# Performance work log

Measured on AMD Instinct MI355X. Metric: run time of the kernel, lower is better.

Reference implementation:

```python
import jax, jax.numpy as jnp
import numpy as np

EPS = 1e-7  # tf.keras.backend.epsilon()
ITERATIONS = 3

def squash(t, axis=-1):
    n2 = jnp.sum(jnp.square(t), axis=axis, keepdims=True)
    scale = n2 / (1.0 + n2) / jnp.sqrt(n2 + EPS)
    return scale * t

def setup_inputs() -> dict:
    key = jax.random.key(0)
    k1, k2 = jax.random.split(key)
    B, N_in, K_in = 64, 1152, 8
    N_out, K_out = 64, 16
    x = jax.random.normal(k1, (B, N_in, K_in), dtype=jnp.float32)
    W = jax.random.normal(k2, (N_out, N_in, K_out, K_in), dtype=jnp.float32) * 0.05
    return {"x": x, "W": W}

def reference(x, W):
    # x: [B, N_in, K_in]; W: [N_out, N_in, K_out, K_in]
    # prediction vectors u: [B, N_out, N_in, K_out]
    u = jnp.einsum('oikj,bij->boik', W, x)
    B, N_out, N_in, K_out = u.shape
    b = jnp.zeros((B, N_out, N_in), dtype=u.dtype)
    v = None
    for i in range(ITERATIONS):
        c = jax.nn.softmax(b, axis=1)            # softmax over N_out
        s = jnp.einsum('boi,boik->bok', c, u)    # [B, N_out, K_out]
        v = squash(s, axis=-1)
        if i < ITERATIONS - 1:
            b = b + jnp.einsum('bok,boik->boi', v, u)
    return v  # [B, N_out, K_out]
```

## Files before the change

kernel.cpp:

```cpp
#include <hip/hip_runtime.h>
#include <math.h>


#define CTI 18
#define IPB 2
#define NSTEP 9
#define CNCH 64

typedef __attribute__((ext_vector_type(8))) short short8v;
typedef __attribute__((ext_vector_type(8))) unsigned short ushort8v;
typedef __attribute__((ext_vector_type(4))) float f32x4;

typedef const __attribute__((address_space(1))) unsigned int gu32;
typedef __attribute__((address_space(3))) unsigned int lu32;

__device__ __forceinline__ unsigned short f2bf(float f) {
    unsigned u = __builtin_bit_cast(unsigned, f);
    u = u + 0x7FFFu + ((u >> 16) & 1u);
    return (unsigned short)(u >> 16);
}
__device__ __forceinline__ float bf2f(unsigned short h) {
    unsigned u = ((unsigned)h) << 16;
    return __builtin_bit_cast(float, u);
}
__device__ __forceinline__ float lo16f(unsigned u) {
    return __builtin_bit_cast(float, u << 16);
}
__device__ __forceinline__ float hi16f(unsigned u) {
    return __builtin_bit_cast(float, u & 0xFFFF0000u);
}

__global__ __launch_bounds__(256)
void xform(const float* __restrict__ W, const float* __restrict__ x,
           unsigned short* __restrict__ Wp, unsigned short* __restrict__ xpp) {
    const int bid = blockIdx.x;
    if (bid < 4608) {
        int tid = bid * 256 + threadIdx.x;
        int k = tid & 15, o = (tid >> 4) & 63, i = tid >> 10;
        const float4* src = (const float4*)(W + (((size_t)o * 1152 + i) * 16 + k) * 8);
        float4 v0 = src[0], v1 = src[1];
        float vf[8] = {v0.x, v0.y, v0.z, v0.w, v1.x, v1.y, v1.z, v1.w};
        ushort8v hi, lo;
        #pragma unroll
        for (int j = 0; j < 8; ++j) {
            unsigned short h = f2bf(vf[j]);
            hi[j] = h;
            lo[j] = f2bf(vf[j] - bf2f(h));
        }
        size_t base = (((size_t)i * 64 + o) * 2) * 128 + (size_t)k * 8;
        *reinterpret_cast<ushort8v*>(Wp + base)       = hi;
        *reinterpret_cast<ushort8v*>(Wp + base + 128) = lo;
    } else {
        int tid = (bid - 4608) * 256 + threadIdx.x;
        int b = tid & 63, i = tid >> 6;
        const float4* src = (const float4*)(x + ((size_t)b * 1152 + i) * 8);
        float4 v0 = src[0], v1 = src[1];
        float vf[8] = {v0.x, v0.y, v0.z, v0.w, v1.x, v1.y, v1.z, v1.w};
        ushort8v hi, lo;
        #pragma unroll
        for (int j = 0; j < 8; ++j) {
            unsigned short h = f2bf(vf[j]);
            hi[j] = h;
            lo[j] = f2bf(vf[j] - bf2f(h));
        }
        size_t base = ((size_t)i * 2) * 512 + (size_t)b * 8;
        *reinterpret_cast<ushort8v*>(xpp + base)       = hi;
        *reinterpret_cast<ushort8v*>(xpp + base + 512) = lo;
    }
}

template<int ROUTED>
__global__ __launch_bounds__(1024, 1)
void caps_mfma(const unsigned short* __restrict__ Wp,
               const unsigned short* __restrict__ xp,
               const float* __restrict__ Vfp,
               unsigned short* __restrict__ spart) {
    __shared__ unsigned short wlds[2][IPB * 16384];
    __shared__ float zbuf[2][IPB][256];

    const int t = threadIdx.x;
    const int wv = t >> 6, l = t & 63;
    const int btile = blockIdx.x >> 6, chunk = blockIdx.x & 63;
    const int g = l >> 4, b15 = l & 15;
    const int o0 = wv * 4;
    const int i0 = chunk * CTI;

    uint2 vpk[4];
    if (ROUTED) {
        #pragma unroll
        for (int oo = 0; oo < 4; ++oo) {
            f32x4 Vf = *reinterpret_cast<const f32x4*>(
                Vfp + (((size_t)btile * 64 + o0 + oo) * 64 + l) * 4);
            vpk[oo].x = (unsigned)f2bf(Vf[0]) | ((unsigned)f2bf(Vf[1]) << 16);
            vpk[oo].y = (unsigned)f2bf(Vf[2]) | ((unsigned)f2bf(Vf[3]) << 16);
        }
    }

    f32x4 s[4];
    #pragma unroll
    for (int oo = 0; oo < 4; ++oo) s[oo] = (f32x4){0.f, 0.f, 0.f, 0.f};

    #define STAGE2(buf, ibase)                                                    \
    {                                                                             \
        const ushort8v* srcb = reinterpret_cast<const ushort8v*>(                 \
            Wp + (size_t)(ibase) * 16384);                                        \
        _Pragma("unroll")                                                         \
        for (int r = 0; r < 4; ++r)                                               \
            __builtin_amdgcn_global_load_lds(                                     \
                (gu32*)(srcb + (r * 1024 + wv * 64 + l)),                         \
                (lu32*)&wlds[buf][(size_t)(r * 1024 + wv * 64) * 8], 16, 0, 0);   \
    }

    #define LOADB(i) (*reinterpret_cast<const short8v*>(                          \
        xp + (((size_t)(i) * 2 + (l >> 5)) * 64 + btile * 16 + b15) * 8))

    STAGE2(0, i0);
    short8v Bf0 = LOADB(i0);
    short8v Bf1 = LOADB(i0 + 1);
    __syncthreads();

    int cur = 0;
    for (int st = 0; st < NSTEP; ++st) {
        short8v Bn0 = Bf0, Bn1 = Bf1;
        if (st + 1 < NSTEP) {
            STAGE2(cur ^ 1, i0 + (st + 1) * IPB);
            Bn0 = LOADB(i0 + (st + 1) * IPB);
            Bn1 = LOADB(i0 + (st + 1) * IPB + 1);
        }

        if (!ROUTED) {
            #pragma unroll
            for (int oo = 0; oo < 4; ++oo) {
                short8v Af0 = *reinterpret_cast<const short8v*>(
                    &wlds[cur][0] + (((o0 + oo) * 2 + (g & 1)) * 128 + b15 * 8));
                s[oo] = __builtin_amdgcn_mfma_f32_16x16x32_bf16(Af0, Bf0, s[oo], 0, 0, 0);
                short8v Af1 = *reinterpret_cast<const short8v*>(
                    &wlds[cur][16384] + (((o0 + oo) * 2 + (g & 1)) * 128 + b15 * 8));
                s[oo] = __builtin_amdgcn_mfma_f32_16x16x32_bf16(Af1, Bf1, s[oo], 0, 0, 0);
            }
            __syncthreads();
        } else {
            f32x4 u[IPB][4];
            float lg[IPB][4];
            float Zp0 = 0.f, Zp1 = 0.f;
            #pragma unroll
            for (int oo = 0; oo < 4; ++oo) {
                short8v Af0 = *reinterpret_cast<const short8v*>(
                    &wlds[cur][0] + (((o0 + oo) * 2 + (g & 1)) * 128 + b15 * 8));
                f32x4 zz = {0.f, 0.f, 0.f, 0.f};
                u[0][oo] = __builtin_amdgcn_mfma_f32_16x16x32_bf16(Af0, Bf0, zz, 0, 0, 0);
                short8v Af1 = *reinterpret_cast<const short8v*>(
                    &wlds[cur][16384] + (((o0 + oo) * 2 + (g & 1)) * 128 + b15 * 8));
                u[1][oo] = __builtin_amdgcn_mfma_f32_16x16x32_bf16(Af1, Bf1, zz, 0, 0, 0);

                float p0 = u[0][oo][0] * lo16f(vpk[oo].x);
                p0 = fmaf(u[0][oo][1], hi16f(vpk[oo].x), p0);
                p0 = fmaf(u[0][oo][2], lo16f(vpk[oo].y), p0);
                p0 = fmaf(u[0][oo][3], hi16f(vpk[oo].y), p0);
                float p1 = u[1][oo][0] * lo16f(vpk[oo].x);
                p1 = fmaf(u[1][oo][1], hi16f(vpk[oo].x), p1);
                p1 = fmaf(u[1][oo][2], lo16f(vpk[oo].y), p1);
                p1 = fmaf(u[1][oo][3], hi16f(vpk[oo].y), p1);
                p0 += __shfl_xor(p0, 16, 64);  p1 += __shfl_xor(p1, 16, 64);
                p0 += __shfl_xor(p0, 32, 64);  p1 += __shfl_xor(p1, 32, 64);
                float e0 = __expf(p0), e1 = __expf(p1);
                lg[0][oo] = e0; lg[1][oo] = e1;
                Zp0 += e0; Zp1 += e1;
            }
            if (l < 16) {
                zbuf[st & 1][0][wv * 16 + l] = Zp0;
                zbuf[st & 1][1][wv * 16 + l] = Zp1;
            }
            __syncthreads();
            float Z0 = zbuf[st & 1][0][b15];
            float Z1 = zbuf[st & 1][1][b15];
            #pragma unroll
            for (int w2 = 1; w2 < 16; ++w2) {
                Z0 += zbuf[st & 1][0][w2 * 16 + b15];
                Z1 += zbuf[st & 1][1][w2 * 16 + b15];
            }
            float rz0 = 1.0f / Z0, rz1 = 1.0f / Z1;
            #pragma unroll
            for (int oo = 0; oo < 4; ++oo) {
                float c0 = lg[0][oo] * rz0;
                float c1 = lg[1][oo] * rz1;
                s[oo][0] = fmaf(c0, u[0][oo][0], fmaf(c1, u[1][oo][0], s[oo][0]));
                s[oo][1] = fmaf(c0, u[0][oo][1], fmaf(c1, u[1][oo][1], s[oo][1]));
                s[oo][2] = fmaf(c0, u[0][oo][2], fmaf(c1, u[1][oo][2], s[oo][2]));
                s[oo][3] = fmaf(c0, u[0][oo][3], fmaf(c1, u[1][oo][3], s[oo][3]));
            }
        }
        Bf0 = Bn0; Bf1 = Bn1;
        cur ^= 1;
    }

    const float fin = ROUTED ? 1.0f : (1.0f / 64.0f);
    #pragma unroll
    for (int oo = 0; oo < 4; ++oo) {
        f32x4 vv = s[oo] * fin;
        uint2 pk;
        pk.x = (unsigned)f2bf(vv[0]) | ((unsigned)f2bf(vv[1]) << 16);
        pk.y = (unsigned)f2bf(vv[2]) | ((unsigned)f2bf(vv[3]) << 16);
        *reinterpret_cast<uint2*>(spart +
            ((((size_t)chunk * 4 + btile) * 64 + (o0 + oo)) * 64 + l) * 4) = pk;
    }
    #undef STAGE2
    #undef LOADB
}

template<int MODE>
__global__ __launch_bounds__(256)
void reduce2(const unsigned short* __restrict__ spart, float* __restrict__ Vfp,
             float* __restrict__ out) {
    __shared__ f32x4 red[256];
    const int t = threadIdx.x;
    const int l = t & 63, cq = t >> 6;
    const int pair = blockIdx.x;
    const int btile = pair >> 6, o = pair & 63;

    f32x4 acc = {0.f, 0.f, 0.f, 0.f};
    const unsigned short* base = spart + (((size_t)btile * 64 + o) * 64 + l) * 4;
    for (int c = cq * (CNCH/4); c < (cq + 1) * (CNCH/4); ++c) {
        uint2 w = *reinterpret_cast<const uint2*>(base + (size_t)c * 65536);
        acc[0] += lo16f(w.x); acc[1] += hi16f(w.x);
        acc[2] += lo16f(w.y); acc[3] += hi16f(w.y);
    }
    red[t] = acc;
    __syncthreads();
    if (cq == 0) {
        acc = red[l] + red[64 + l] + red[128 + l] + red[192 + l];
        float n2 = acc[0]*acc[0] + acc[1]*acc[1] + acc[2]*acc[2] + acc[3]*acc[3];
        n2 += __shfl_xor(n2, 16, 64);
        n2 += __shfl_xor(n2, 32, 64);
        const float scale = n2 / (1.0f + n2) / sqrtf(n2 + 1e-7f);
        f32x4 v = acc * scale;
        float* vp = Vfp + (((size_t)btile * 64 + o) * 64 + l) * 4;
        if (MODE == 0) {
            *reinterpret_cast<f32x4*>(vp) = v;
        } else if (MODE == 1) {
            f32x4 old = *reinterpret_cast<const f32x4*>(vp);
            *reinterpret_cast<f32x4*>(vp) = old + v;
        } else {
            const int b = btile * 16 + (l & 15), gq = l >> 4;
            *reinterpret_cast<f32x4*>(out + (((size_t)b * 64 + o) * 16 + gq * 4)) = v;
        }
    }
}

#define FTI 18
#define FNCH 64

__device__ __forceinline__ void load_lds16(const float4* gp, float4* lp) {
    __builtin_amdgcn_global_load_lds((gu32*)gp, (lu32*)lp, 16, 0, 0);
}
__device__ __forceinline__ float rfl(float v) {
    return __builtin_bit_cast(float, __builtin_amdgcn_readfirstlane(__builtin_bit_cast(int, v)));
}

template<bool UNIFORM>
__global__ __launch_bounds__(256, 2)
void caps_route_fb(const float* __restrict__ x, const float* __restrict__ W,
                   const float* __restrict__ Vsum, float* __restrict__ s_out) {
    __shared__ float4 wlds[2][2048];
    __shared__ float4 xlds[8 * FTI * 2];
    const int t = threadIdx.x;
    const int w = t >> 6, o = t & 63;
    const int chunk = blockIdx.x % FNCH, bblk = blockIdx.x / FNCH;
    const int i0 = chunk * FTI, bbase = bblk * 8 + w * 2;
    const float4* __restrict__ xg = (const float4*)x;
    const float4* __restrict__ Wg = (const float4*)W;
    for (int e = t; e < 8 * FTI * 2; e += 256) {
        int bb = e / (FTI * 2), r = e % (FTI * 2);
        xlds[e] = xg[((bblk * 8 + bb) * 1152 + i0 + (r >> 1)) * 2 + (r & 1)];
    }
    const float4* wsrc = Wg + (size_t)o * 36864 + (size_t)i0 * 32 + w * 8;
    #pragma unroll
    for (int r = 0; r < 8; ++r) load_lds16(wsrc + r, &wlds[0][(w * 8 + r) * 64]);
    float vsf[2][16];
    if (!UNIFORM) {
        const float4* vg = (const float4*)Vsum;
        #pragma unroll
        for (int ll = 0; ll < 2; ++ll)
            #pragma unroll
            for (int q = 0; q < 4; ++q) {
                float4 v = vg[((size_t)(bbase + ll) * 64 + o) * 4 + q];
                vsf[ll][q*4+0] = v.x; vsf[ll][q*4+1] = v.y;
                vsf[ll][q*4+2] = v.z; vsf[ll][q*4+3] = v.w;
            }
    }
    float sacc[2][16];
    #pragma unroll
    for (int ll = 0; ll < 2; ++ll)
        #pragma unroll
        for (int k = 0; k < 16; ++k) sacc[ll][k] = 0.0f;
    for (int ii = 0; ii < FTI; ++ii) {
        const int cur = ii & 1;
        __syncthreads();
        if (ii + 1 < FTI) {
            const float4* ws = wsrc + (size_t)(ii + 1) * 32;
            #pragma unroll
            for (int r = 0; r < 8; ++r) load_lds16(ws + r, &wlds[cur ^ 1][(w * 8 + r) * 64]);
        }
        float4 A0 = xlds[(w*2+0)*(FTI*2) + ii*2 + 0];
        float4 B0 = xlds[(w*2+0)*(FTI*2) + ii*2 + 1];
        float4 A1 = xlds[(w*2+1)*(FTI*2) + ii*2 + 0];
        float4 B1 = xlds[(w*2+1)*(FTI*2) + ii*2 + 1];
        float xa0x=rfl(A0.x),xa0y=rfl(A0.y),xa0z=rfl(A0.z),xa0w=rfl(A0.w);
        float xb0x=rfl(B0.x),xb0y=rfl(B0.y),xb0z=rfl(B0.z),xb0w=rfl(B0.w);
        float xa1x=rfl(A1.x),xa1y=rfl(A1.y),xa1z=rfl(A1.z),xa1w=rfl(A1.w);
        float xb1x=rfl(B1.x),xb1y=rfl(B1.y),xb1z=rfl(B1.z),xb1w=rfl(B1.w);
        const float4* wb = wlds[cur];
        float u[2][16];
        float logit0 = 0.0f, logit1 = 0.0f;
        #pragma unroll
        for (int k = 0; k < 16; ++k) {
            float4 w0 = wb[(2*k  )*64 + o];
            float4 w1 = wb[(2*k+1)*64 + o];
            float uk0 = w0.x*xa0x; uk0=fmaf(w0.y,xa0y,uk0); uk0=fmaf(w0.z,xa0z,uk0);
            uk0=fmaf(w0.w,xa0w,uk0); uk0=fmaf(w1.x,xb0x,uk0); uk0=fmaf(w1.y,xb0y,uk0);
            uk0=fmaf(w1.z,xb0z,uk0); uk0=fmaf(w1.w,xb0w,uk0);
            float uk1 = w0.x*xa1x; uk1=fmaf(w0.y,xa1y,uk1); uk1=fmaf(w0.z,xa1z,uk1);
            uk1=fmaf(w0.w,xa1w,uk1); uk1=fmaf(w1.x,xb1x,uk1); uk1=fmaf(w1.y,xb1y,uk1);
            uk1=fmaf(w1.z,xb1z,uk1); uk1=fmaf(w1.w,xb1w,uk1);
            u[0][k]=uk0; u[1][k]=uk1;
            if (!UNIFORM) { logit0=fmaf(vsf[0][k],uk0,logit0); logit1=fmaf(vsf[1][k],uk1,logit1); }
        }
        float c0, c1;
        if (UNIFORM) { c0 = c1 = 1.0f/64.0f; }
        else {
            float m0=logit0, m1=logit1;
            #pragma unroll
            for (int d=32; d>=1; d>>=1) { m0=fmaxf(m0,__shfl_xor(m0,d,64)); m1=fmaxf(m1,__shfl_xor(m1,d,64)); }
            float e0=__expf(logit0-m0), e1=__expf(logit1-m1);
            float s0=e0, s1=e1;
            #pragma unroll
            for (int d=32; d>=1; d>>=1) { s0+=__shfl_xor(s0,d,64); s1+=__shfl_xor(s1,d,64); }
            c0=e0/s0; c1=e1/s1;
        }
        #pragma unroll
        for (int k = 0; k < 16; ++k) {
            sacc[0][k]=fmaf(c0,u[0][k],sacc[0][k]);
            sacc[1][k]=fmaf(c1,u[1][k],sacc[1][k]);
        }
    }
    #pragma unroll
    for (int ll = 0; ll < 2; ++ll) {
        float4* sp = (float4*)s_out + (((size_t)chunk * 64 + (bbase + ll)) * 64 + o) * 4;
        sp[0]=make_float4(sacc[ll][0],sacc[ll][1],sacc[ll][2],sacc[ll][3]);
        sp[1]=make_float4(sacc[ll][4],sacc[ll][5],sacc[ll][6],sacc[ll][7]);
        sp[2]=make_float4(sacc[ll][8],sacc[ll][9],sacc[ll][10],sacc[ll][11]);
        sp[3]=make_float4(sacc[ll][12],sacc[ll][13],sacc[ll][14],sacc[ll][15]);
    }
}

template<int MODE>
__global__ __launch_bounds__(256)
void reduce_squash_fb(const float* __restrict__ sp, float* __restrict__ Vs, float* __restrict__ out) {
    const int t = threadIdx.x;
    const int p = t >> 4, q = t & 15;
    const int pair = blockIdx.x * 16 + p;
    const int b = pair >> 6, o = pair & 63;
    float acc[16];
    #pragma unroll
    for (int k = 0; k < 16; ++k) acc[k] = 0.0f;
    const float4* base = (const float4*)sp;
    for (int c = q * (FNCH/16); c < (q + 1) * (FNCH/16); ++c) {
        const float4* pptr = base + (((size_t)c * 64 + b) * 64 + o) * 4;
        float4 v0=pptr[0],v1=pptr[1],v2=pptr[2],v3=pptr[3];
        acc[0]+=v0.x;acc[1]+=v0.y;acc[2]+=v0.z;acc[3]+=v0.w;
        acc[4]+=v1.x;acc[5]+=v1.y;acc[6]+=v1.z;acc[7]+=v1.w;
        acc[8]+=v2.x;acc[9]+=v2.y;acc[10]+=v2.z;acc[11]+=v2.w;
        acc[12]+=v3.x;acc[13]+=v3.y;acc[14]+=v3.z;acc[15]+=v3.w;
    }
    #pragma unroll
    for (int d = 1; d < 16; d <<= 1)
        #pragma unroll
        for (int k = 0; k < 16; ++k) acc[k] += __shfl_xor(acc[k], d, 64);
    if (q == 0) {
        float n2 = 0.0f;
        #pragma unroll
        for (int k = 0; k < 16; ++k) n2 = fmaf(acc[k], acc[k], n2);
        const float scale = n2 / (1.0f + n2) / sqrtf(n2 + 1e-7f);
        if (MODE == 0) {
            float4* vf = (float4*)Vs + (size_t)pair * 4;
            #pragma unroll
            for (int r = 0; r < 4; ++r)
                vf[r] = make_float4(scale*acc[r*4+0],scale*acc[r*4+1],scale*acc[r*4+2],scale*acc[r*4+3]);
        } else if (MODE == 1) {
            float4* vf = (float4*)Vs + (size_t)pair * 4;
            #pragma unroll
            for (int r = 0; r < 4; ++r) {
                float4 v = vf[r];
                v.x=fmaf(scale,acc[r*4+0],v.x); v.y=fmaf(scale,acc[r*4+1],v.y);
                v.z=fmaf(scale,acc[r*4+2],v.z); v.w=fmaf(scale,acc[r*4+3],v.w);
                vf[r] = v;
            }
        } else {
            float4* of = (float4*)out + (size_t)pair * 4;
            #pragma unroll
            for (int r = 0; r < 4; ++r)
                of[r] = make_float4(scale*acc[r*4+0],scale*acc[r*4+1],scale*acc[r*4+2],scale*acc[r*4+3]);
        }
    }
}

extern "C" void kernel_launch(void* const* d_in, const int* in_sizes, int n_in,
                              void* d_out, int out_size, void* d_ws, size_t ws_size,
                              hipStream_t stream) {
    const float* x = (const float*)d_in[0];
    const float* W = (const float*)d_in[1];
    float* out = (float*)d_out;

    float* Vfp = (float*)d_ws;
    unsigned short* spart = (unsigned short*)(Vfp + 65536);
    unsigned short* Wp = spart + (size_t)CNCH * 65536;
    unsigned short* xpp = Wp + (size_t)1152 * 64 * 256;
    const size_t need_full = (size_t)65536 * 4
        + ((size_t)CNCH * 65536 + (size_t)1152 * 64 * 256 + (size_t)1152 * 2 * 512) * 2;

    if (ws_size >= need_full) {
        xform<<<4608 + 288, 256, 0, stream>>>(W, x, Wp, xpp);
        caps_mfma<0><<<256, 1024, 0, stream>>>(Wp, xpp, Vfp, spart);
        reduce2<0><<<256, 256, 0, stream>>>(spart, Vfp, out);
        caps_mfma<1><<<256, 1024, 0, stream>>>(Wp, xpp, Vfp, spart);
        reduce2<1><<<256, 256, 0, stream>>>(spart, Vfp, out);
        caps_mfma<1><<<256, 1024, 0, stream>>>(Wp, xpp, Vfp, spart);
        reduce2<2><<<256, 256, 0, stream>>>(spart, Vfp, out);
    } else {
        float* Vs = (float*)d_ws;
        float* sp = Vs + 65536;
        dim3 grid(8 * FNCH), blk(256);
        dim3 rg(256), rb(256);
        caps_route_fb<true ><<<grid, blk, 0, stream>>>(x, W, nullptr, sp);
        reduce_squash_fb<0><<<rg, rb, 0, stream>>>(sp, Vs, out);
        caps_route_fb<false><<<grid, blk, 0, stream>>>(x, W, Vs, sp);
        reduce_squash_fb<1><<<rg, rb, 0, stream>>>(sp, Vs, out);
        caps_route_fb<false><<<grid, blk, 0, stream>>>(x, W, Vs, sp);
        reduce_squash_fb<2><<<rg, rb, 0, stream>>>(sp, Vs, out);
    }
}
```

Baseline: 91.49 us.

## Fuse all routing passes into one cooperative kernel with grid syncs

Measured after the change: 309.4 us. 3.38x slower.

```diff
diff --git a/kernel.cpp b/kernel.cpp
--- a/kernel.cpp
+++ b/kernel.cpp
@@ -1,5 +1,8 @@
 #include <hip/hip_runtime.h>
+#include <hip/hip_cooperative_groups.h>
 #include <math.h>
+
+namespace cg = cooperative_groups;
 
 
 #define CTI 18
@@ -28,6 +31,230 @@
 }
 __device__ __forceinline__ float hi16f(unsigned u) {
     return __builtin_bit_cast(float, u & 0xFFFF0000u);
+}
+
+__global__ __launch_bounds__(1024, 1)
+void caps_fused(const float* __restrict__ W, const float* __restrict__ x,
+                unsigned short* __restrict__ Wp, unsigned short* __restrict__ xp,
+                float* __restrict__ Vfp, unsigned short* __restrict__ spart,
+                float* __restrict__ out) {
+    cg::grid_group grid = cg::this_grid();
+
+    __shared__ alignas(16) unsigned short wlds[2][IPB * 16384];
+    __shared__ float zbuf[2][IPB][256];
+
+    const int t = threadIdx.x;
+    const int wv = t >> 6, l = t & 63;
+    const int btile = blockIdx.x >> 6, chunk = blockIdx.x & 63;
+    const int g = l >> 4, b15 = l & 15;
+    const int o0 = wv * 4;
+    const int i0 = chunk * CTI;
+
+    {
+        const int gtid = blockIdx.x * 1024 + t;
+        for (int idx = gtid; idx < 1152 * 64 * 16; idx += 256 * 1024) {
+            int k = idx & 15, o = (idx >> 4) & 63, i = idx >> 10;
+            const float4* src = (const float4*)(W + (((size_t)o * 1152 + i) * 16 + k) * 8);
+            float4 v0 = src[0], v1 = src[1];
+            float vf[8] = {v0.x, v0.y, v0.z, v0.w, v1.x, v1.y, v1.z, v1.w};
+            ushort8v hi, lo;
+            #pragma unroll
+            for (int j = 0; j < 8; ++j) {
+                unsigned short h = f2bf(vf[j]);
+                hi[j] = h;
+                lo[j] = f2bf(vf[j] - bf2f(h));
+            }
+            size_t base = (((size_t)i * 64 + o) * 2) * 128 + (size_t)k * 8;
+            *reinterpret_cast<ushort8v*>(Wp + base)       = hi;
+            *reinterpret_cast<ushort8v*>(Wp + base + 128) = lo;
+        }
+        for (int idx = gtid; idx < 1152 * 64; idx += 256 * 1024) {
+            int b = idx & 63, i = idx >> 6;
+            const float4* src = (const float4*)(x + ((size_t)b * 1152 + i) * 8);
+            float4 v0 = src[0], v1 = src[1];
+            float vf[8] = {v0.x, v0.y, v0.z, v0.w, v1.x, v1.y, v1.z, v1.w};
+            ushort8v hi, lo;
+            #pragma unroll
+            for (int j = 0; j < 8; ++j) {
+                unsigned short h = f2bf(vf[j]);
+                hi[j] = h;
+                lo[j] = f2bf(vf[j] - bf2f(h));
+            }
+            size_t base = ((size_t)i * 2) * 512 + (size_t)b * 8;
+            *reinterpret_cast<ushort8v*>(xp + base)       = hi;
+            *reinterpret_cast<ushort8v*>(xp + base + 512) = lo;
+        }
+    }
+
+    #define STAGE2(buf, ibase)                                                    \
+    {                                                                             \
+        const ushort8v* srcb = reinterpret_cast<const ushort8v*>(                 \
+            Wp + (size_t)(ibase) * 16384);                                        \
+        _Pragma("unroll")                                                         \
+        for (int r = 0; r < 4; ++r)                                               \
+            __builtin_amdgcn_global_load_lds(                                     \
+                (gu32*)(srcb + (r * 1024 + wv * 64 + l)),                         \
+                (lu32*)&wlds[buf][(size_t)(r * 1024 + wv * 64) * 8], 16, 0, 0);   \
+    }
+    #define LOADB(i) (*reinterpret_cast<const short8v*>(                          \
+        xp + (((size_t)(i) * 2 + (l >> 5)) * 64 + btile * 16 + b15) * 8))
+
+    #define CAPS_PASS(R)                                                          \
+    {                                                                             \
+        uint2 vpk[4];                                                             \
+        if (R) {                                                                  \
+            _Pragma("unroll")                                                     \
+            for (int oo = 0; oo < 4; ++oo) {                                      \
+                f32x4 Vf = *reinterpret_cast<const f32x4*>(                       \
+                    Vfp + (((size_t)btile * 64 + o0 + oo) * 64 + l) * 4);         \
+                vpk[oo].x = (unsigned)f2bf(Vf[0]) | ((unsigned)f2bf(Vf[1]) << 16);\
+                vpk[oo].y = (unsigned)f2bf(Vf[2]) | ((unsigned)f2bf(Vf[3]) << 16);\
+            }                                                                     \
+        }                                                                         \
+        f32x4 s[4];                                                               \
+        _Pragma("unroll")                                                         \
+        for (int oo = 0; oo < 4; ++oo) s[oo] = (f32x4){0.f, 0.f, 0.f, 0.f};       \
+        STAGE2(0, i0);                                                            \
+        short8v Bf0 = LOADB(i0);                                                  \
+        short8v Bf1 = LOADB(i0 + 1);                                              \
+        __syncthreads();                                                          \
+        int cur = 0;                                                              \
+        for (int st = 0; st < NSTEP; ++st) {                                      \
+            short8v Bn0 = Bf0, Bn1 = Bf1;                                         \
+            if (st + 1 < NSTEP) {                                                 \
+                STAGE2(cur ^ 1, i0 + (st + 1) * IPB);                             \
+                Bn0 = LOADB(i0 + (st + 1) * IPB);                                 \
+                Bn1 = LOADB(i0 + (st + 1) * IPB + 1);                             \
+            }                                                                     \
+            if (!R) {                                                             \
+                _Pragma("unroll")                                                 \
+                for (int oo = 0; oo < 4; ++oo) {                                  \
+                    short8v Af0 = *reinterpret_cast<const short8v*>(              \
+                        &wlds[cur][0] + (((o0+oo)*2 + (g&1))*128 + b15*8));       \
+                    s[oo] = __builtin_amdgcn_mfma_f32_16x16x32_bf16(Af0, Bf0, s[oo], 0, 0, 0); \
+                    short8v Af1 = *reinterpret_cast<const short8v*>(              \
+                        &wlds[cur][16384] + (((o0+oo)*2 + (g&1))*128 + b15*8));   \
+                    s[oo] = __builtin_amdgcn_mfma_f32_16x16x32_bf16(Af1, Bf1, s[oo], 0, 0, 0); \
+                }                                                                 \
+                __syncthreads();                                                  \
+            } else {                                                              \
+                f32x4 u[IPB][4];                                                  \
+                float lg[IPB][4];                                                 \
+                float Zp0 = 0.f, Zp1 = 0.f;                                       \
+                _Pragma("unroll")                                                 \
+                for (int oo = 0; oo < 4; ++oo) {                                  \
+                    short8v Af0 = *reinterpret_cast<const short8v*>(              \
+                        &wlds[cur][0] + (((o0+oo)*2 + (g&1))*128 + b15*8));       \
+                    f32x4 zz = {0.f, 0.f, 0.f, 0.f};                              \
+                    u[0][oo] = __builtin_amdgcn_mfma_f32_16x16x32_bf16(Af0, Bf0, zz, 0, 0, 0); \
+                    short8v Af1 = *reinterpret_cast<const short8v*>(              \
+                        &wlds[cur][16384] + (((o0+oo)*2 + (g&1))*128 + b15*8));   \
+                    u[1][oo] = __builtin_amdgcn_mfma_f32_16x16x32_bf16(Af1, Bf1, zz, 0, 0, 0); \
+                    float p0 = u[0][oo][0] * lo16f(vpk[oo].x);                    \
+                    p0 = fmaf(u[0][oo][1], hi16f(vpk[oo].x), p0);                 \
+                    p0 = fmaf(u[0][oo][2], lo16f(vpk[oo].y), p0);                 \
+                    p0 = fmaf(u[0][oo][3], hi16f(vpk[oo].y), p0);                 \
+                    float p1 = u[1][oo][0] * lo16f(vpk[oo].x);                    \
+                    p1 = fmaf(u[1][oo][1], hi16f(vpk[oo].x), p1);                 \
+                    p1 = fmaf(u[1][oo][2], lo16f(vpk[oo].y), p1);                 \
+                    p1 = fmaf(u[1][oo][3], hi16f(vpk[oo].y), p1);                 \
+                    p0 += __shfl_xor(p0, 16, 64);  p1 += __shfl_xor(p1, 16, 64);  \
+                    p0 += __shfl_xor(p0, 32, 64);  p1 += __shfl_xor(p1, 32, 64);  \
+                    float e0 = __expf(p0), e1 = __expf(p1);                       \
+                    lg[0][oo] = e0; lg[1][oo] = e1;                               \
+                    Zp0 += e0; Zp1 += e1;                                         \
+                }                                                                 \
+                if (l < 16) {                                                     \
+                    zbuf[st & 1][0][wv * 16 + l] = Zp0;                           \
+                    zbuf[st & 1][1][wv * 16 + l] = Zp1;                           \
+                }                                                                 \
+                __syncthreads();                                                  \
+                float Z0 = zbuf[st & 1][0][b15];                                  \
+                float Z1 = zbuf[st & 1][1][b15];                                  \
+                _Pragma("unroll")                                                 \
+                for (int w2 = 1; w2 < 16; ++w2) {                                 \
+                    Z0 += zbuf[st & 1][0][w2 * 16 + b15];                         \
+                    Z1 += zbuf[st & 1][1][w2 * 16 + b15];                         \
+                }                                                                 \
+                float rz0 = 1.0f / Z0, rz1 = 1.0f / Z1;                           \
+                _Pragma("unroll")                                                 \
+                for (int oo = 0; oo < 4; ++oo) {                                  \
+                    float c0 = lg[0][oo] * rz0;                                   \
+                    float c1 = lg[1][oo] * rz1;                                   \
+                    s[oo][0] = fmaf(c0, u[0][oo][0], fmaf(c1, u[1][oo][0], s[oo][0])); \
+                    s[oo][1] = fmaf(c0, u[0][oo][1], fmaf(c1, u[1][oo][1], s[oo][1])); \
+                    s[oo][2] = fmaf(c0, u[0][oo][2], fmaf(c1, u[1][oo][2], s[oo][2])); \
+                    s[oo][3] = fmaf(c0, u[0][oo][3], fmaf(c1, u[1][oo][3], s[oo][3])); \
+                }                                                                 \
+            }                                                                     \
+            Bf0 = Bn0; Bf1 = Bn1;                                                 \
+            cur ^= 1;                                                             \
+        }                                                                         \
+        const float fin = (R) ? 1.0f : (1.0f / 64.0f);                            \
+        _Pragma("unroll")                                                         \
+        for (int oo = 0; oo < 4; ++oo) {                                          \
+            f32x4 vv = s[oo] * fin;                                               \
+            uint2 pk;                                                             \
+            pk.x = (unsigned)f2bf(vv[0]) | ((unsigned)f2bf(vv[1]) << 16);         \
+            pk.y = (unsigned)f2bf(vv[2]) | ((unsigned)f2bf(vv[3]) << 16);         \
+            *reinterpret_cast<uint2*>(spart +                                     \
+                ((((size_t)chunk * 4 + btile) * 64 + (o0 + oo)) * 64 + l) * 4) = pk; \
+        }                                                                         \
+    }
+
+    #define REDUCE_PHASE(MODE)                                                    \
+    {                                                                             \
+        f32x4* red = reinterpret_cast<f32x4*>(&wlds[0][0]);                       \
+        const int cq = t >> 6;                                                    \
+        const int pair = blockIdx.x;                                              \
+        const int rb = pair >> 6, ro = pair & 63;                                 \
+        f32x4 acc = {0.f, 0.f, 0.f, 0.f};                                         \
+        const unsigned short* rbase = spart + (((size_t)rb * 64 + ro) * 64 + l) * 4; \
+        for (int c = cq * (CNCH/16); c < (cq + 1) * (CNCH/16); ++c) {             \
+            uint2 w_ = *reinterpret_cast<const uint2*>(rbase + (size_t)c * 65536);\
+            acc[0] += lo16f(w_.x); acc[1] += hi16f(w_.x);                         \
+            acc[2] += lo16f(w_.y); acc[3] += hi16f(w_.y);                         \
+        }                                                                         \
+        red[t] = acc;                                                             \
+        __syncthreads();                                                          \
+        if (cq == 0) {                                                            \
+            _Pragma("unroll")                                                     \
+            for (int w2 = 1; w2 < 16; ++w2) acc += red[w2 * 64 + l];              \
+            float n2 = acc[0]*acc[0] + acc[1]*acc[1] + acc[2]*acc[2] + acc[3]*acc[3]; \
+            n2 += __shfl_xor(n2, 16, 64);                                         \
+            n2 += __shfl_xor(n2, 32, 64);                                         \
+            const float scale = n2 / (1.0f + n2) / sqrtf(n2 + 1e-7f);             \
+            f32x4 v = acc * scale;                                                \
+            float* vp = Vfp + (((size_t)rb * 64 + ro) * 64 + l) * 4;              \
+            if (MODE == 0) {                                                      \
+                *reinterpret_cast<f32x4*>(vp) = v;                                \
+            } else if (MODE == 1) {                                               \
+                f32x4 old = *reinterpret_cast<const f32x4*>(vp);                  \
+                *reinterpret_cast<f32x4*>(vp) = old + v;                          \
+            } else {                                                              \
+                const int b_ = rb * 16 + (l & 15), gq = l >> 4;                   \
+                *reinterpret_cast<f32x4*>(out + (((size_t)b_ * 64 + ro) * 16 + gq * 4)) = v; \
+            }                                                                     \
+        }                                                                         \
+    }
+
+    grid.sync();
+    CAPS_PASS(0)
+    grid.sync();
+    REDUCE_PHASE(0)
+    grid.sync();
+    CAPS_PASS(1)
+    grid.sync();
+    REDUCE_PHASE(1)
+    grid.sync();
+    CAPS_PASS(1)
+    grid.sync();
+    REDUCE_PHASE(2)
+
+    #undef STAGE2
+    #undef LOADB
+    #undef CAPS_PASS
+    #undef REDUCE_PHASE
 }
 
 __global__ __launch_bounds__(256)
@@ -77,14 +304,12 @@
                unsigned short* __restrict__ spart) {
     __shared__ unsigned short wlds[2][IPB * 16384];
     __shared__ float zbuf[2][IPB][256];
-
     const int t = threadIdx.x;
     const int wv = t >> 6, l = t & 63;
     const int btile = blockIdx.x >> 6, chunk = blockIdx.x & 63;
     const int g = l >> 4, b15 = l & 15;
     const int o0 = wv * 4;
     const int i0 = chunk * CTI;
-
     uint2 vpk[4];
     if (ROUTED) {
         #pragma unroll
@@ -95,11 +320,9 @@
             vpk[oo].y = (unsigned)f2bf(Vf[2]) | ((unsigned)f2bf(Vf[3]) << 16);
         }
     }
-
     f32x4 s[4];
     #pragma unroll
     for (int oo = 0; oo < 4; ++oo) s[oo] = (f32x4){0.f, 0.f, 0.f, 0.f};
-
     #define STAGE2(buf, ibase)                                                    \
     {                                                                             \
         const ushort8v* srcb = reinterpret_cast<const ushort8v*>(                 \
@@ -110,15 +333,12 @@
                 (gu32*)(srcb + (r * 1024 + wv * 64 + l)),                         \
                 (lu32*)&wlds[buf][(size_t)(r * 1024 + wv * 64) * 8], 16, 0, 0);   \
     }
-
     #define LOADB(i) (*reinterpret_cast<const short8v*>(                          \
         xp + (((size_t)(i) * 2 + (l >> 5)) * 64 + btile * 16 + b15) * 8))
-
     STAGE2(0, i0);
     short8v Bf0 = LOADB(i0);
     short8v Bf1 = LOADB(i0 + 1);
     __syncthreads();
-
     int cur = 0;
     for (int st = 0; st < NSTEP; ++st) {
         short8v Bn0 = Bf0, Bn1 = Bf1;
@@ -127,7 +347,6 @@
             Bn0 = LOADB(i0 + (st + 1) * IPB);
             Bn1 = LOADB(i0 + (st + 1) * IPB + 1);
         }
-
         if (!ROUTED) {
             #pragma unroll
             for (int oo = 0; oo < 4; ++oo) {
@@ -152,7 +371,6 @@
                 short8v Af1 = *reinterpret_cast<const short8v*>(
                     &wlds[cur][16384] + (((o0 + oo) * 2 + (g & 1)) * 128 + b15 * 8));
                 u[1][oo] = __builtin_amdgcn_mfma_f32_16x16x32_bf16(Af1, Bf1, zz, 0, 0, 0);
-
                 float p0 = u[0][oo][0] * lo16f(vpk[oo].x);
                 p0 = fmaf(u[0][oo][1], hi16f(vpk[oo].x), p0);
                 p0 = fmaf(u[0][oo][2], lo16f(vpk[oo].y), p0);
@@ -193,7 +411,6 @@
         Bf0 = Bn0; Bf1 = Bn1;
         cur ^= 1;
     }
-
     const float fin = ROUTED ? 1.0f : (1.0f / 64.0f);
     #pragma unroll
     for (int oo = 0; oo < 4; ++oo) {
@@ -217,7 +434,6 @@
     const int l = t & 63, cq = t >> 6;
     const int pair = blockIdx.x;
     const int btile = pair >> 6, o = pair & 63;
-
     f32x4 acc = {0.f, 0.f, 0.f, 0.f};
     const unsigned short* base = spart + (((size_t)btile * 64 + o) * 64 + l) * 4;
     for (int c = cq * (CNCH/4); c < (cq + 1) * (CNCH/4); ++c) {
@@ -419,13 +635,20 @@
         + ((size_t)CNCH * 65536 + (size_t)1152 * 64 * 256 + (size_t)1152 * 2 * 512) * 2;
 
     if (ws_size >= need_full) {
-        xform<<<4608 + 288, 256, 0, stream>>>(W, x, Wp, xpp);
-        caps_mfma<0><<<256, 1024, 0, stream>>>(Wp, xpp, Vfp, spart);
-        reduce2<0><<<256, 256, 0, stream>>>(spart, Vfp, out);
-        caps_mfma<1><<<256, 1024, 0, stream>>>(Wp, xpp, Vfp, spart);
-        reduce2<1><<<256, 256, 0, stream>>>(spart, Vfp, out);
-        caps_mfma<1><<<256, 1024, 0, stream>>>(Wp, xpp, Vfp, spart);
-        reduce2<2><<<256, 256, 0, stream>>>(spart, Vfp, out);
+        void* kargs[] = {(void*)&W, (void*)&x, (void*)&Wp, (void*)&xpp,
+                         (void*)&Vfp, (void*)&spart, (void*)&out};
+        hipError_t err = hipLaunchCooperativeKernel((const void*)caps_fused,
+                                                    dim3(256), dim3(1024),
+                                                    kargs, 0, stream);
+        if (err != hipSuccess) {
+            xform<<<4608 + 288, 256, 0, stream>>>(W, x, Wp, xpp);
+            caps_mfma<0><<<256, 1024, 0, stream>>>(Wp, xpp, Vfp, spart);
+            reduce2<0><<<256, 256, 0, stream>>>(spart, Vfp, out);
+            caps_mfma<1><<<256, 1024, 0, stream>>>(Wp, xpp, Vfp, spart);
+            reduce2<1><<<256, 256, 0, stream>>>(spart, Vfp, out);
+            caps_mfma<1><<<256, 1024, 0, stream>>>(Wp, xpp, Vfp, spart);
+            reduce2<2><<<256, 256, 0, stream>>>(spart, Vfp, out);
+        }
     } else {
         float* Vs = (float*)d_ws;
         float* sp = Vs + 65536;
```
